# Performance work log

Measured on AMD Instinct MI355X. Metric: run time of the kernel, lower is better.

The kernel has to match this reference:

```python
import jax, jax.numpy as jnp
import numpy as np

# ---- module constants (from init_kwargs / zounds.SR22050) ----
SEQ = 64
N_SAMPLES = 16384
N_EVENTS = 16
N_HARM = 32
NOISE_WS = 512
NOISE_STEP = 256
NYQ = 11025.0  # SR22050 nyquist
MIN_F0 = 20.0 / NYQ
MAX_F0 = 800.0 / NYQ
F0_DIFF = MAX_F0 - MIN_F0
HARM_FACTOR = jnp.arange(2, 2 + N_HARM, dtype=jnp.float32)  # [2..33]


def lin_interp(x, size):
    """torch F.interpolate(mode='linear', align_corners=False) along last dim."""
    L = x.shape[-1]
    pos = (jnp.arange(size, dtype=x.dtype) + 0.5) * (L / size) - 0.5
    pos = jnp.clip(pos, 0.0, L - 1)
    i0 = jnp.floor(pos).astype(jnp.int32)
    i1 = jnp.minimum(i0 + 1, L - 1)
    w = (pos - i0).astype(x.dtype)
    return x[..., i0] * (1.0 - w) + x[..., i1] * w


def band_filtered_noise(noise_frames, mean, std):
    """Per-frame Gaussian band-pass of white noise in the STFT domain, overlap-add.
    noise_frames: (b,e,F,ws); mean/std: (b,e,F) in normalized freq [0,1]."""
    ws = noise_frames.shape[-1]
    n = jnp.arange(ws, dtype=noise_frames.dtype)
    win = 0.5 - 0.5 * jnp.cos(2.0 * jnp.pi * n / ws)  # Hann
    spec = jnp.fft.rfft(noise_frames * win, axis=-1)  # (b,e,F,ws//2+1)
    freqs = jnp.linspace(0.0, 1.0, ws // 2 + 1)
    filt = jnp.exp(-0.5 * ((freqs[None, None, None, :] - mean[..., None]) / std[..., None]) ** 2)
    frames = jnp.fft.irfft(spec * filt, n=ws, axis=-1)  # (b,e,F,ws)
    # overlap-add with hop NOISE_STEP (ws == 2*step -> two half-chunks per frame)
    b, e, Fn, _ = frames.shape
    chunks = frames.reshape(b, e, Fn, 2, NOISE_STEP)
    a = chunks[..., 0, :].reshape(b, e, Fn * NOISE_STEP)
    c = chunks[..., 1, :].reshape(b, e, Fn * NOISE_STEP)
    out = jnp.zeros((b, e, (Fn + 1) * NOISE_STEP), dtype=frames.dtype)
    out = out.at[..., : Fn * NOISE_STEP].add(a)
    out = out.at[..., NOISE_STEP:].add(c)
    return out[..., :N_SAMPLES]


def setup_inputs() -> dict:
    key = jax.random.key(0)
    ks = jax.random.split(key, 8)
    B = 8
    return {
        "f0": jax.random.uniform(ks[0], (B, N_EVENTS, SEQ), jnp.float32),
        "overall_env": jax.random.uniform(ks[1], (B, N_EVENTS, SEQ), jnp.float32),
        "osc_env": jax.random.uniform(ks[2], (B, N_EVENTS, SEQ), jnp.float32),
        "noise_env": jax.random.uniform(ks[3], (B, N_EVENTS, SEQ), jnp.float32),
        "harm_env": jax.random.uniform(ks[4], (B, N_EVENTS, N_HARM, SEQ), jnp.float32),
        "noise_std": jax.random.uniform(ks[5], (B, N_EVENTS, SEQ), jnp.float32),
        "f0_baselines": jax.random.uniform(ks[6], (B, N_EVENTS, 1), jnp.float32),
        "noise_frames": jax.random.normal(ks[7], (B, N_EVENTS, SEQ, NOISE_WS), jnp.float32),
    }


def reference(f0, overall_env, osc_env, noise_env, harm_env, noise_std, f0_baselines, noise_frames):
    # f0_baselines branch (ERB-scaled deviation around baseline)
    f0 = jnp.clip(f0, -0.5, 0.5)
    scaled_erb = (0.108 * (f0_baselines * NYQ) + 24.7) / NYQ
    f0 = f0_baselines + f0 * scaled_erb

    orig_f0 = f0 = jnp.clip(f0, 0.0, 1.0)
    overall_env = jnp.clip(overall_env, 0.0, 1.0)
    osc_env = jnp.clip(osc_env, 0.0, 1.0)
    harm_env = jnp.clip(harm_env, 0.0, 1.0)
    noise_std = jnp.clip(noise_std, 1e-12, 1.0)

    f0n = MIN_F0 + f0 * F0_DIFF                                   # (b,e,S)
    harm_f = f0n[:, :, None, :] * HARM_FACTOR[None, None, :, None]  # (b,e,H,S)
    harm_env = osc_env[:, :, None, :] * harm_env                  # (b,e,H,S)

    fund = lin_interp(f0n, N_SAMPLES)           # (b,e,N)
    harm_f_i = lin_interp(harm_f, N_SAMPLES)    # (b,e,H,N)
    osc_env_i = lin_interp(osc_env, N_SAMPLES)  # (b,e,N)
    harm_env_i = lin_interp(harm_env, N_SAMPLES)

    fundamental = jnp.sin(jnp.cumsum(fund * jnp.pi, axis=-1)) * osc_env_i
    harmonics = (jnp.sin(jnp.cumsum(harm_f_i * jnp.pi, axis=-1)) * harm_env_i).sum(axis=-2)
    osc = fundamental + harmonics

    noise_mean = MIN_F0 + orig_f0 * F0_DIFF
    nstd = noise_std * F0_DIFF
    noise = band_filtered_noise(noise_frames, noise_mean, nstd)

    osc_mix = lin_interp(overall_env, N_SAMPLES)
    noise_mix = lin_interp(1.0 - overall_env, N_SAMPLES)
    return osc * osc_mix + noise * noise_mix
```

## Files before the change

### kernel.cpp

```cpp
#include <hip/hip_runtime.h>
#include <math.h>

#define SEQ 64
#define NSAMP 16384
#define NHARM 32
#define NWS 512
#define NSTEP 256
#define BE 128
#define NFRAMES 8192

typedef _Float16 half8 __attribute__((ext_vector_type(8)));
typedef float f32x4 __attribute__((ext_vector_type(4)));

__device__ __forceinline__ float sin_rev(float x) {
  float r; asm("v_sin_f32 %0, %1" : "=v"(r) : "v"(x)); return r;
}
__device__ __forceinline__ float cos_rev(float x) {
  float r; asm("v_cos_f32 %0, %1" : "=v"(r) : "v"(x)); return r;
}
__device__ __forceinline__ float clip01(float v) { return fminf(fmaxf(v, 0.0f), 1.0f); }

__device__ __forceinline__ float f0_to_norm(float f0v, float bl) {
  const float NYQ = 11025.0f;
  const float MIN_F0 = 20.0f / 11025.0f;
  const float F0_DIFF = 780.0f / 11025.0f;
  float v = fminf(fmaxf(f0v, -0.5f), 0.5f);
  float erb = (0.108f * (bl * NYQ) + 24.7f) / NYQ;
  float fv = clip01(bl + v * erb);
  return MIN_F0 + fv * F0_DIFF;
}

__global__ __launch_bounds__(256) void prep_k(_Float16* __restrict__ W1) {
  const int m = blockIdx.x, k = m & 127;
  const int tid = threadIdx.x;
  const bool isSin = m >= 128;
  for (int n = tid; n < 512; n += 256) {
    int a = (k * n) & 511;
    float ph = (float)a * (1.0f / 512.0f);
    W1[m * 512 + n] = (_Float16)(isSin ? sin_rev(ph) : cos_rev(ph));
  }
}

__global__ __launch_bounds__(256) void gemmf_k(const float* __restrict__ Af,
                                               const _Float16* __restrict__ B,
                                               _Float16* __restrict__ Cout,
                                               _Float16* __restrict__ W2,
                                               const float* __restrict__ f0,
                                               const float* __restrict__ nstd,
                                               const float* __restrict__ f0b) {
  const int tid = threadIdx.x;

  if (blockIdx.x < 256) {
    const int k = tid & 127;
    const bool isSin = tid >= 128;
#pragma unroll
    for (int rr = 0; rr < 2; ++rr) {
      const int n = blockIdx.x * 2 + rr;
      int a = (k * n) & 511;
      float ph = (float)a * (1.0f / 512.0f);
      W2[n * 256 + tid] = (_Float16)(isSin ? sin_rev(ph) : cos_rev(ph));
    }
    return;
  }

  const int p = blockIdx.x - 256;
  const int x = p & 7, j = p >> 3;
  const int mstripe = ((j >> 2) << 3) + x;
  const int bn0 = (j & 3) * 64;
  const int m0 = mstripe * 64;

  const int Kt = 512;
  const int wave = tid >> 6, lane = tid & 63;
  const int r = lane & 15, q = lane >> 4;
  __shared__ __align__(16) _Float16 Ash[2][64 * 64];
  __shared__ __align__(16) _Float16 Bsh[2][64 * 64];
  __shared__ __align__(16) float whann[512];

  const int nT = Kt >> 6;
  const int srow0 = tid >> 3, srow1 = (256 + tid) >> 3;
  const int skg = tid & 7;

  half8 ra[2], rb[2];
  f32x4 acc[4] = {};

  whann[tid] = 0.5f - 0.5f * cos_rev((float)tid * (1.0f / 512.0f));
  whann[tid + 256] = 0.5f - 0.5f * cos_rev((float)(tid + 256) * (1.0f / 512.0f));
  __syncthreads();

  auto load_a = [&](int kk) {
    const float* s0 = Af + (size_t)(m0 + srow0) * Kt + kk + skg * 8;
    const float* s1 = Af + (size_t)(m0 + srow1) * Kt + kk + skg * 8;
    float4 a0 = ((const float4*)s0)[0], a1 = ((const float4*)s0)[1];
    float4 b0 = ((const float4*)s1)[0], b1 = ((const float4*)s1)[1];
    float4 w0 = *(const float4*)(&whann[kk + skg * 8]);
    float4 w1 = *(const float4*)(&whann[kk + skg * 8 + 4]);
    ra[0][0] = (_Float16)(a0.x * w0.x); ra[0][1] = (_Float16)(a0.y * w0.y);
    ra[0][2] = (_Float16)(a0.z * w0.z); ra[0][3] = (_Float16)(a0.w * w0.w);
    ra[0][4] = (_Float16)(a1.x * w1.x); ra[0][5] = (_Float16)(a1.y * w1.y);
    ra[0][6] = (_Float16)(a1.z * w1.z); ra[0][7] = (_Float16)(a1.w * w1.w);
    ra[1][0] = (_Float16)(b0.x * w0.x); ra[1][1] = (_Float16)(b0.y * w0.y);
    ra[1][2] = (_Float16)(b0.z * w0.z); ra[1][3] = (_Float16)(b0.w * w0.w);
    ra[1][4] = (_Float16)(b1.x * w1.x); ra[1][5] = (_Float16)(b1.y * w1.y);
    ra[1][6] = (_Float16)(b1.z * w1.z); ra[1][7] = (_Float16)(b1.w * w1.w);
    rb[0] = *(const half8*)(B + (size_t)(bn0 + srow0) * Kt + kk + skg * 8);
    rb[1] = *(const half8*)(B + (size_t)(bn0 + srow1) * Kt + kk + skg * 8);
  };
  auto store_lds = [&](int b) {
    *(half8*)(&Ash[b][srow0 * 64 + ((skg ^ (srow0 & 7)) << 3)]) = ra[0];
    *(half8*)(&Ash[b][srow1 * 64 + ((skg ^ (srow1 & 7)) << 3)]) = ra[1];
    *(half8*)(&Bsh[b][srow0 * 64 + ((skg ^ (srow0 & 7)) << 3)]) = rb[0];
    *(half8*)(&Bsh[b][srow1 * 64 + ((skg ^ (srow1 & 7)) << 3)]) = rb[1];
  };

  load_a(0);
  store_lds(0);

  for (int t = 0;;) {
    if (t + 1 < nT) load_a((t + 1) << 6);
    __syncthreads();
    const int b = t & 1;
#pragma unroll
    for (int ks = 0; ks < 2; ++ks) {
      const int swz = ((ks * 4 + q) ^ (r & 7)) << 3;
      half8 af = *(const half8*)(&Ash[b][(wave * 16 + r) * 64 + swz]);
      half8 bf0 = *(const half8*)(&Bsh[b][(0 * 16 + r) * 64 + swz]);
      half8 bf1 = *(const half8*)(&Bsh[b][(1 * 16 + r) * 64 + swz]);
      half8 bf2 = *(const half8*)(&Bsh[b][(2 * 16 + r) * 64 + swz]);
      half8 bf3 = *(const half8*)(&Bsh[b][(3 * 16 + r) * 64 + swz]);
      acc[0] = __builtin_amdgcn_mfma_f32_16x16x32_f16(af, bf0, acc[0], 0, 0, 0);
      acc[1] = __builtin_amdgcn_mfma_f32_16x16x32_f16(af, bf1, acc[1], 0, 0, 0);
      acc[2] = __builtin_amdgcn_mfma_f32_16x16x32_f16(af, bf2, acc[2], 0, 0, 0);
      acc[3] = __builtin_amdgcn_mfma_f32_16x16x32_f16(af, bf3, acc[3], 0, 0, 0);
    }
    if (t + 1 >= nT) break;
    __syncthreads();
    store_lds((t + 1) & 1);
    ++t;
  }

  const float F0_DIFF = 780.0f / 11025.0f;
#pragma unroll
  for (int reg = 0; reg < 4; ++reg) {
    const int row = m0 + wave * 16 + q * 4 + reg;
    const float mu = f0_to_norm(f0[row], f0b[row >> 6]);
    const float sd = fminf(fmaxf(nstd[row], 1e-12f), 1.0f) * F0_DIFF;
    const float inv_sd = 1.0f / sd;
    const float a = inv_sd * (1.0f / 256.0f);
    const float bmu = mu * inv_sd;
#pragma unroll
    for (int ni = 0; ni < 4; ++ni) {
      const int col = bn0 + ni * 16 + r;
      const int k = col & 127;
      float z = fmaf((float)k, a, -bmu);
      float cf = (k == 0) ? (1.0f / 512.0f) : (2.0f / 512.0f);
      float s = cf * exp2f(z * z * -0.72134752044f);
      Cout[(size_t)row * 256 + col] = (_Float16)(acc[ni][reg] * s);
    }
  }
}

__global__ __launch_bounds__(256) void invfin_k(const _Float16* __restrict__ AB,
                                                const _Float16* __restrict__ W2,
                                                const float* __restrict__ f0,
                                                const float* __restrict__ f0b,
                                                const float* __restrict__ oenv_g,
                                                const float* __restrict__ oscenv_g,
                                                const float* __restrict__ henv_g,
                                                float* __restrict__ out) {
  const int p = blockIdx.x;
  const int x = p & 7, j = p >> 3;
  const int be = ((j >> 2) << 3) + x;
  const int n0 = (j & 3) * 64;
  const int m0 = be * 64;
  const int tid = threadIdx.x;
  const int wave = tid >> 6, lane = tid & 63;
  const int r = lane & 15, q = lane >> 4;

  __shared__ __align__(16) _Float16 Ash[65 * 64];
  __shared__ __align__(16) _Float16 B1sh[64 * 64];
  __shared__ __align__(16) _Float16 B2sh[64 * 64];
  __shared__ __align__(16) float4 qe4[8 * SEQ];
  __shared__ float oenv[SEQ], oscE[SEQ];
  __shared__ float Fs[SEQ], Ds[SEQ], Gs[SEQ];

  if (tid < SEQ) {
    oenv[tid] = clip01(oenv_g[be * SEQ + tid]);
    oscE[tid] = clip01(oscenv_g[be * SEQ + tid]);
    Fs[tid] = f0_to_norm(f0[be * SEQ + tid], f0b[be]);
  }
  __syncthreads();

  if (tid < SEQ) {
    const int s = tid;
    float fcur = Fs[s];
    float fnxt = (s < 63) ? Fs[s + 1] : Fs[63];
    Ds[s] = fnxt - fcur;
    double term = 128.0 * ((double)fcur + (double)fnxt);
    double sc = term;
#pragma unroll
    for (int off = 1; off < 64; off <<= 1) {
      double u = __shfl_up(sc, off, 64);
      if (s >= off) sc += u;
    }
    double C = 128.0 * (double)Fs[0] + (sc - term);
    Gs[s] = (float)(C - 2.0 * floor(C * 0.5));
  }

  for (int idx = tid; idx < 8 * SEQ; idx += 256) {
    int hq = idx >> 6, s = idx & 63;
    const float* hb = henv_g + (size_t)be * (NHARM * SEQ) + (4 * hq) * SEQ + s;
    float e = oscE[s];
    qe4[idx] = make_float4(e * clip01(hb[0]), e * clip01(hb[64]),
                           e * clip01(hb[128]), e * clip01(hb[192]));
  }

  auto stage_AB = [&](int kk) {
#pragma unroll
    for (int it = 0; it < 3; ++it) {
      int g = it * 256 + tid;
      if (g < 520) {
        int row = g >> 3, kg = g & 7;
        half8 v = {0, 0, 0, 0, 0, 0, 0, 0};
        if (row > 0)
          v = *(const half8*)(AB + (size_t)(m0 - 1 + row) * 256 + kk + kg * 8);
        *(half8*)(&Ash[row * 64 + ((kg ^ (row & 7)) << 3)]) = v;
      }
    }
#pragma unroll
    for (int it = 0; it < 4; ++it) {
      int g = it * 256 + tid;
      int row = (g >> 3) & 63, kg = g & 7;
      bool second = g >= 512;
      int wrow = n0 + row + (second ? 256 : 0);
      half8 v = *(const half8*)(W2 + (size_t)wrow * 256 + kk + kg * 8);
      _Float16* dst = second ? B2sh : B1sh;
      *(half8*)(&dst[row * 64 + ((kg ^ (row & 7)) << 3)]) = v;
    }
  };

  f32x4 acc[4] = {};
  stage_AB(0);
  __syncthreads();

  for (int t = 0;;) {
#pragma unroll
    for (int ks = 0; ks < 2; ++ks) {
      const int kg = ks * 4 + q;
      const int ra1 = 1 + wave * 16 + r;
      const int ra2 = wave * 16 + r;
      half8 af1 = *(const half8*)(&Ash[ra1 * 64 + ((kg ^ (ra1 & 7)) << 3)]);
      half8 af2 = *(const half8*)(&Ash[ra2 * 64 + ((kg ^ (ra2 & 7)) << 3)]);
#pragma unroll
      for (int ni = 0; ni < 4; ++ni) {
        const int rb = ni * 16 + r;
        const int sw = (kg ^ (rb & 7)) << 3;
        half8 bf1 = *(const half8*)(&B1sh[rb * 64 + sw]);
        half8 bf2 = *(const half8*)(&B2sh[rb * 64 + sw]);
        acc[ni] = __builtin_amdgcn_mfma_f32_16x16x32_f16(af1, bf1, acc[ni], 0, 0, 0);
        acc[ni] = __builtin_amdgcn_mfma_f32_16x16x32_f16(af2, bf2, acc[ni], 0, 0, 0);
      }
    }
    if (t == 3) break;
    __syncthreads();
    stage_AB((t + 1) << 6);
    __syncthreads();
    ++t;
  }

#pragma unroll
  for (int reg = 0; reg < 4; ++reg) {
    const int c = wave * 16 + q * 4 + reg;
#pragma unroll
    for (int ni = 0; ni < 4; ++ni) {
      const int n = n0 + ni * 16 + r;
      const int t = c * 256 + n;
      float pos = ((float)t + 0.5f) * (1.0f / 256.0f) - 0.5f;
      pos = fminf(fmaxf(pos, 0.0f), 63.0f);
      int i0 = (int)pos;
      int i1 = min(i0 + 1, 63);
      float w = pos - (float)i0;

      float pph;
      if (t < 128) {
        pph = (float)(t + 1) * Fs[0];
      } else {
        int s = (t - 128) >> 8;
        float u1 = (float)((t - 128) - (s << 8) + 1);
        pph = Gs[s] + fmaf(Ds[s] * (1.0f / 512.0f), u1 * u1, u1 * Fs[s]);
      }
      pph = pph - 2.0f * floorf(pph * 0.5f);
      float xv = pph * 0.5f;
      float sb = sin_rev(xv);
      float cb = cos_rev(xv);
      float C = 2.0f * cb;

      float fund = sb * (oscE[i0] * (1.0f - w) + oscE[i1] * w);
      float d0 = 0.0f, d1 = 0.0f;
      float sp = sb;
      float scur = C * sb;
#pragma unroll
      for (int hq = 0; hq < 8; ++hq) {
        float4 qa = qe4[hq * 64 + i0];
        float4 qb = qe4[hq * 64 + i1];
        d0 = fmaf(scur, qa.x, d0); d1 = fmaf(scur, qb.x, d1);
        sp = fmaf(C, scur, -sp);
        d0 = fmaf(sp, qa.y, d0);   d1 = fmaf(sp, qb.y, d1);
        scur = fmaf(C, sp, -scur);
        d0 = fmaf(scur, qa.z, d0); d1 = fmaf(scur, qb.z, d1);
        sp = fmaf(C, scur, -sp);
        d0 = fmaf(sp, qa.w, d0);   d1 = fmaf(sp, qb.w, d1);
        scur = fmaf(C, sp, -scur);
      }
      float osc = fund + d0 * (1.0f - w) + d1 * w;
      float mix = oenv[i0] * (1.0f - w) + oenv[i1] * w;
      out[(size_t)be * NSAMP + t] = fmaf(osc, mix, acc[ni][reg] * (1.0f - mix));
    }
  }
}

extern "C" void kernel_launch(void* const* d_in, const int* in_sizes, int n_in,
                              void* d_out, int out_size, void* d_ws, size_t ws_size,
                              hipStream_t stream) {
  const float* f0           = (const float*)d_in[0];
  const float* overall_env  = (const float*)d_in[1];
  const float* osc_env      = (const float*)d_in[2];
  const float* harm_env     = (const float*)d_in[4];
  const float* noise_std    = (const float*)d_in[5];
  const float* f0_base      = (const float*)d_in[6];
  const float* noise_frames = (const float*)d_in[7];
  float* out = (float*)d_out;

  _Float16* W1 = (_Float16*)d_ws;
  _Float16* W2 = W1 + 256 * 512;
  _Float16* AB = W2 + 512 * 256;

  prep_k<<<256, 256, 0, stream>>>(W1);
  gemmf_k<<<768, 256, 0, stream>>>(noise_frames, W1, AB, W2, f0, noise_std, f0_base);
  invfin_k<<<512, 256, 0, stream>>>(
      AB, W2, f0, f0_base, overall_env, osc_env, harm_env, out);
}
```

Baseline: 36.95 us.

## Fuse three kernels into one monolithic kernel with on-the-fly DFT twiddles

Replaces the prep, forward-DFT GEMM and inverse/finalize kernels with a single kernel in which each block handles 8 output chunks plus a halo frame. The forward spectrum is kept in shared memory instead of a global intermediate. DFT twiddle factors are generated in registers with hardware sin/cos rather than loaded from precomputed tables. This removes two launches and the global round-trips, but adds much transcendental work per MFMA and recomputes the halo frame, and the M dimension of each 16-row MFMA tile is only partly used (10 of 16 rows).

```diff
diff --git a/kernel.cpp b/kernel.cpp
--- a/kernel.cpp
+++ b/kernel.cpp
@@ -4,8 +4,6 @@
 #define SEQ 64
 #define NSAMP 16384
 #define NHARM 32
-#define NWS 512
-#define NSTEP 256
 #define BE 128
 #define NFRAMES 8192
 
@@ -30,163 +28,42 @@
   return MIN_F0 + fv * F0_DIFF;
 }
 
-__global__ __launch_bounds__(256) void prep_k(_Float16* __restrict__ W1) {
-  const int m = blockIdx.x, k = m & 127;
-  const int tid = threadIdx.x;
-  const bool isSin = m >= 128;
-  for (int n = tid; n < 512; n += 256) {
-    int a = (k * n) & 511;
-    float ph = (float)a * (1.0f / 512.0f);
-    W1[m * 512 + n] = (_Float16)(isSin ? sin_rev(ph) : cos_rev(ph));
-  }
-}
-
-__global__ __launch_bounds__(256) void gemmf_k(const float* __restrict__ Af,
-                                               const _Float16* __restrict__ B,
-                                               _Float16* __restrict__ Cout,
-                                               _Float16* __restrict__ W2,
-                                               const float* __restrict__ f0,
-                                               const float* __restrict__ nstd,
-                                               const float* __restrict__ f0b) {
-  const int tid = threadIdx.x;
-
-  if (blockIdx.x < 256) {
-    const int k = tid & 127;
-    const bool isSin = tid >= 128;
-#pragma unroll
-    for (int rr = 0; rr < 2; ++rr) {
-      const int n = blockIdx.x * 2 + rr;
-      int a = (k * n) & 511;
-      float ph = (float)a * (1.0f / 512.0f);
-      W2[n * 256 + tid] = (_Float16)(isSin ? sin_rev(ph) : cos_rev(ph));
-    }
-    return;
-  }
-
-  const int p = blockIdx.x - 256;
-  const int x = p & 7, j = p >> 3;
-  const int mstripe = ((j >> 2) << 3) + x;
-  const int bn0 = (j & 3) * 64;
-  const int m0 = mstripe * 64;
-
-  const int Kt = 512;
-  const int wave = tid >> 6, lane = tid & 63;
-  const int r = lane & 15, q = lane >> 4;
-  __shared__ __align__(16) _Float16 Ash[2][64 * 64];
-  __shared__ __align__(16) _Float16 Bsh[2][64 * 64];
+__global__ __launch_bounds__(256, 4) void mono_k(
+    const float* __restrict__ Af,
+    const float* __restrict__ f0,
+    const float* __restrict__ nstd,
+    const float* __restrict__ f0b,
+    const float* __restrict__ oenv_g,
+    const float* __restrict__ oscenv_g,
+    const float* __restrict__ henv_g,
+    float* __restrict__ out) {
+  __shared__ __align__(16) _Float16 A_all[10 * 512];
+  __shared__ __align__(16) _Float16 ABl[10 * 256];
   __shared__ __align__(16) float whann[512];
-
-  const int nT = Kt >> 6;
-  const int srow0 = tid >> 3, srow1 = (256 + tid) >> 3;
-  const int skg = tid & 7;
-
-  half8 ra[2], rb[2];
-  f32x4 acc[4] = {};
-
-  whann[tid] = 0.5f - 0.5f * cos_rev((float)tid * (1.0f / 512.0f));
-  whann[tid + 256] = 0.5f - 0.5f * cos_rev((float)(tid + 256) * (1.0f / 512.0f));
-  __syncthreads();
-
-  auto load_a = [&](int kk) {
-    const float* s0 = Af + (size_t)(m0 + srow0) * Kt + kk + skg * 8;
-    const float* s1 = Af + (size_t)(m0 + srow1) * Kt + kk + skg * 8;
-    float4 a0 = ((const float4*)s0)[0], a1 = ((const float4*)s0)[1];
-    float4 b0 = ((const float4*)s1)[0], b1 = ((const float4*)s1)[1];
-    float4 w0 = *(const float4*)(&whann[kk + skg * 8]);
-    float4 w1 = *(const float4*)(&whann[kk + skg * 8 + 4]);
-    ra[0][0] = (_Float16)(a0.x * w0.x); ra[0][1] = (_Float16)(a0.y * w0.y);
-    ra[0][2] = (_Float16)(a0.z * w0.z); ra[0][3] = (_Float16)(a0.w * w0.w);
-    ra[0][4] = (_Float16)(a1.x * w1.x); ra[0][5] = (_Float16)(a1.y * w1.y);
-    ra[0][6] = (_Float16)(a1.z * w1.z); ra[0][7] = (_Float16)(a1.w * w1.w);
-    ra[1][0] = (_Float16)(b0.x * w0.x); ra[1][1] = (_Float16)(b0.y * w0.y);
-    ra[1][2] = (_Float16)(b0.z * w0.z); ra[1][3] = (_Float16)(b0.w * w0.w);
-    ra[1][4] = (_Float16)(b1.x * w1.x); ra[1][5] = (_Float16)(b1.y * w1.y);
-    ra[1][6] = (_Float16)(b1.z * w1.z); ra[1][7] = (_Float16)(b1.w * w1.w);
-    rb[0] = *(const half8*)(B + (size_t)(bn0 + srow0) * Kt + kk + skg * 8);
-    rb[1] = *(const half8*)(B + (size_t)(bn0 + srow1) * Kt + kk + skg * 8);
-  };
-  auto store_lds = [&](int b) {
-    *(half8*)(&Ash[b][srow0 * 64 + ((skg ^ (srow0 & 7)) << 3)]) = ra[0];
-    *(half8*)(&Ash[b][srow1 * 64 + ((skg ^ (srow1 & 7)) << 3)]) = ra[1];
-    *(half8*)(&Bsh[b][srow0 * 64 + ((skg ^ (srow0 & 7)) << 3)]) = rb[0];
-    *(half8*)(&Bsh[b][srow1 * 64 + ((skg ^ (srow1 & 7)) << 3)]) = rb[1];
-  };
-
-  load_a(0);
-  store_lds(0);
-
-  for (int t = 0;;) {
-    if (t + 1 < nT) load_a((t + 1) << 6);
-    __syncthreads();
-    const int b = t & 1;
-#pragma unroll
-    for (int ks = 0; ks < 2; ++ks) {
-      const int swz = ((ks * 4 + q) ^ (r & 7)) << 3;
-      half8 af = *(const half8*)(&Ash[b][(wave * 16 + r) * 64 + swz]);
-      half8 bf0 = *(const half8*)(&Bsh[b][(0 * 16 + r) * 64 + swz]);
-      half8 bf1 = *(const half8*)(&Bsh[b][(1 * 16 + r) * 64 + swz]);
-      half8 bf2 = *(const half8*)(&Bsh[b][(2 * 16 + r) * 64 + swz]);
-      half8 bf3 = *(const half8*)(&Bsh[b][(3 * 16 + r) * 64 + swz]);
-      acc[0] = __builtin_amdgcn_mfma_f32_16x16x32_f16(af, bf0, acc[0], 0, 0, 0);
-      acc[1] = __builtin_amdgcn_mfma_f32_16x16x32_f16(af, bf1, acc[1], 0, 0, 0);
-      acc[2] = __builtin_amdgcn_mfma_f32_16x16x32_f16(af, bf2, acc[2], 0, 0, 0);
-      acc[3] = __builtin_amdgcn_mfma_f32_16x16x32_f16(af, bf3, acc[3], 0, 0, 0);
-    }
-    if (t + 1 >= nT) break;
-    __syncthreads();
-    store_lds((t + 1) & 1);
-    ++t;
-  }
-
-  const float F0_DIFF = 780.0f / 11025.0f;
-#pragma unroll
-  for (int reg = 0; reg < 4; ++reg) {
-    const int row = m0 + wave * 16 + q * 4 + reg;
-    const float mu = f0_to_norm(f0[row], f0b[row >> 6]);
-    const float sd = fminf(fmaxf(nstd[row], 1e-12f), 1.0f) * F0_DIFF;
-    const float inv_sd = 1.0f / sd;
-    const float a = inv_sd * (1.0f / 256.0f);
-    const float bmu = mu * inv_sd;
-#pragma unroll
-    for (int ni = 0; ni < 4; ++ni) {
-      const int col = bn0 + ni * 16 + r;
-      const int k = col & 127;
-      float z = fmaf((float)k, a, -bmu);
-      float cf = (k == 0) ? (1.0f / 512.0f) : (2.0f / 512.0f);
-      float s = cf * exp2f(z * z * -0.72134752044f);
-      Cout[(size_t)row * 256 + col] = (_Float16)(acc[ni][reg] * s);
-    }
-  }
-}
-
-__global__ __launch_bounds__(256) void invfin_k(const _Float16* __restrict__ AB,
-                                                const _Float16* __restrict__ W2,
-                                                const float* __restrict__ f0,
-                                                const float* __restrict__ f0b,
-                                                const float* __restrict__ oenv_g,
-                                                const float* __restrict__ oscenv_g,
-                                                const float* __restrict__ henv_g,
-                                                float* __restrict__ out) {
+  __shared__ __align__(16) float4 qe4[8 * SEQ];
+  __shared__ float oenv[SEQ], oscE[SEQ], Fs[SEQ], Ds[SEQ], Gs[SEQ];
+
   const int p = blockIdx.x;
-  const int x = p & 7, j = p >> 3;
-  const int be = ((j >> 2) << 3) + x;
-  const int n0 = (j & 3) * 64;
-  const int m0 = be * 64;
+  const int be = p >> 3, qc = p & 7;
+  const int c0 = be * 64 + qc * 8;
   const int tid = threadIdx.x;
   const int wave = tid >> 6, lane = tid & 63;
   const int r = lane & 15, q = lane >> 4;
-
-  __shared__ __align__(16) _Float16 Ash[65 * 64];
-  __shared__ __align__(16) _Float16 B1sh[64 * 64];
-  __shared__ __align__(16) _Float16 B2sh[64 * 64];
-  __shared__ __align__(16) float4 qe4[8 * SEQ];
-  __shared__ float oenv[SEQ], oscE[SEQ];
-  __shared__ float Fs[SEQ], Ds[SEQ], Gs[SEQ];
-
+  const int wc = wave * 64;
+
+  whann[tid] = 0.5f - 0.5f * cos_rev((float)tid * (1.0f / 512.0f));
+  whann[tid + 256] = 0.5f - 0.5f * cos_rev((float)(tid + 256) * (1.0f / 512.0f));
   if (tid < SEQ) {
     oenv[tid] = clip01(oenv_g[be * SEQ + tid]);
     oscE[tid] = clip01(oscenv_g[be * SEQ + tid]);
     Fs[tid] = f0_to_norm(f0[be * SEQ + tid], f0b[be]);
+  }
+  for (int idx = tid; idx < 8 * SEQ; idx += 256) {
+    int hq = idx >> 6, s = idx & 63;
+    const float* hb = henv_g + (size_t)be * (NHARM * SEQ) + (4 * hq) * SEQ + s;
+    float e = clip01(oscenv_g[be * SEQ + s]);
+    qe4[idx] = make_float4(e * clip01(hb[0]), e * clip01(hb[64]),
+                           e * clip01(hb[128]), e * clip01(hb[192]));
   }
   __syncthreads();
 
@@ -205,115 +82,163 @@
     double C = 128.0 * (double)Fs[0] + (sc - term);
     Gs[s] = (float)(C - 2.0 * floor(C * 0.5));
   }
-
-  for (int idx = tid; idx < 8 * SEQ; idx += 256) {
-    int hq = idx >> 6, s = idx & 63;
-    const float* hb = henv_g + (size_t)be * (NHARM * SEQ) + (4 * hq) * SEQ + s;
-    float e = oscE[s];
-    qe4[idx] = make_float4(e * clip01(hb[0]), e * clip01(hb[64]),
-                           e * clip01(hb[128]), e * clip01(hb[192]));
-  }
-
-  auto stage_AB = [&](int kk) {
-#pragma unroll
-    for (int it = 0; it < 3; ++it) {
-      int g = it * 256 + tid;
-      if (g < 520) {
-        int row = g >> 3, kg = g & 7;
-        half8 v = {0, 0, 0, 0, 0, 0, 0, 0};
-        if (row > 0)
-          v = *(const half8*)(AB + (size_t)(m0 - 1 + row) * 256 + kk + kg * 8);
-        *(half8*)(&Ash[row * 64 + ((kg ^ (row & 7)) << 3)]) = v;
-      }
-    }
-#pragma unroll
-    for (int it = 0; it < 4; ++it) {
-      int g = it * 256 + tid;
-      int row = (g >> 3) & 63, kg = g & 7;
-      bool second = g >= 512;
-      int wrow = n0 + row + (second ? 256 : 0);
-      half8 v = *(const half8*)(W2 + (size_t)wrow * 256 + kk + kg * 8);
-      _Float16* dst = second ? B2sh : B1sh;
-      *(half8*)(&dst[row * 64 + ((kg ^ (row & 7)) << 3)]) = v;
-    }
-  };
-
-  f32x4 acc[4] = {};
-  stage_AB(0);
+  for (int g = tid; g < 640; g += 256) {
+    int row = g >> 6, kg = g & 63;
+    half8 v = {0, 0, 0, 0, 0, 0, 0, 0};
+    if (row < 9) {
+      int fi = max(c0 - 1 + row, 0);
+      const float* s0 = Af + (size_t)fi * 512 + kg * 8;
+      float4 a0 = ((const float4*)s0)[0], a1 = ((const float4*)s0)[1];
+      float4 w0 = *(const float4*)(&whann[kg * 8]);
+      float4 w1 = *(const float4*)(&whann[kg * 8 + 4]);
+      v[0] = (_Float16)(a0.x * w0.x); v[1] = (_Float16)(a0.y * w0.y);
+      v[2] = (_Float16)(a0.z * w0.z); v[3] = (_Float16)(a0.w * w0.w);
+      v[4] = (_Float16)(a1.x * w1.x); v[5] = (_Float16)(a1.y * w1.y);
+      v[6] = (_Float16)(a1.z * w1.z); v[7] = (_Float16)(a1.w * w1.w);
+    }
+    *(half8*)(&A_all[row * 512 + ((kg ^ (row & 7)) << 3)]) = v;
+  }
   __syncthreads();
 
-  for (int t = 0;;) {
-#pragma unroll
-    for (int ks = 0; ks < 2; ++ks) {
-      const int kg = ks * 4 + q;
-      const int ra1 = 1 + wave * 16 + r;
-      const int ra2 = wave * 16 + r;
-      half8 af1 = *(const half8*)(&Ash[ra1 * 64 + ((kg ^ (ra1 & 7)) << 3)]);
-      half8 af2 = *(const half8*)(&Ash[ra2 * 64 + ((kg ^ (ra2 & 7)) << 3)]);
+  {
+    f32x4 acc[4] = {};
+    int kW[4]; bool isS[4];
+#pragma unroll
+    for (int ni = 0; ni < 4; ++ni) {
+      int kap = wc + ni * 16 + r;
+      kW[ni] = kap & 127;
+      isS[ni] = kap >= 128;
+    }
+    const int arow = min(r, 9);
+    for (int u = 0; u < 16; ++u) {
+      int g = u * 4 + q;
+      half8 af = *(const half8*)(&A_all[arow * 512 + ((g ^ (arow & 7)) << 3)]);
+      int nb = u * 32 + q * 8;
 #pragma unroll
       for (int ni = 0; ni < 4; ++ni) {
-        const int rb = ni * 16 + r;
-        const int sw = (kg ^ (rb & 7)) << 3;
-        half8 bf1 = *(const half8*)(&B1sh[rb * 64 + sw]);
-        half8 bf2 = *(const half8*)(&B2sh[rb * 64 + sw]);
-        acc[ni] = __builtin_amdgcn_mfma_f32_16x16x32_f16(af1, bf1, acc[ni], 0, 0, 0);
-        acc[ni] = __builtin_amdgcn_mfma_f32_16x16x32_f16(af2, bf2, acc[ni], 0, 0, 0);
-      }
-    }
-    if (t == 3) break;
-    __syncthreads();
-    stage_AB((t + 1) << 6);
-    __syncthreads();
-    ++t;
-  }
-
-#pragma unroll
-  for (int reg = 0; reg < 4; ++reg) {
-    const int c = wave * 16 + q * 4 + reg;
-#pragma unroll
-    for (int ni = 0; ni < 4; ++ni) {
-      const int n = n0 + ni * 16 + r;
-      const int t = c * 256 + n;
-      float pos = ((float)t + 0.5f) * (1.0f / 256.0f) - 0.5f;
-      pos = fminf(fmaxf(pos, 0.0f), 63.0f);
-      int i0 = (int)pos;
-      int i1 = min(i0 + 1, 63);
-      float w = pos - (float)i0;
-
-      float pph;
-      if (t < 128) {
-        pph = (float)(t + 1) * Fs[0];
-      } else {
-        int s = (t - 128) >> 8;
-        float u1 = (float)((t - 128) - (s << 8) + 1);
-        pph = Gs[s] + fmaf(Ds[s] * (1.0f / 512.0f), u1 * u1, u1 * Fs[s]);
-      }
-      pph = pph - 2.0f * floorf(pph * 0.5f);
-      float xv = pph * 0.5f;
-      float sb = sin_rev(xv);
-      float cb = cos_rev(xv);
-      float C = 2.0f * cb;
-
-      float fund = sb * (oscE[i0] * (1.0f - w) + oscE[i1] * w);
-      float d0 = 0.0f, d1 = 0.0f;
-      float sp = sb;
-      float scur = C * sb;
-#pragma unroll
-      for (int hq = 0; hq < 8; ++hq) {
-        float4 qa = qe4[hq * 64 + i0];
-        float4 qb = qe4[hq * 64 + i1];
-        d0 = fmaf(scur, qa.x, d0); d1 = fmaf(scur, qb.x, d1);
-        sp = fmaf(C, scur, -sp);
-        d0 = fmaf(sp, qa.y, d0);   d1 = fmaf(sp, qb.y, d1);
-        scur = fmaf(C, sp, -scur);
-        d0 = fmaf(scur, qa.z, d0); d1 = fmaf(scur, qb.z, d1);
-        sp = fmaf(C, scur, -sp);
-        d0 = fmaf(sp, qa.w, d0);   d1 = fmaf(sp, qb.w, d1);
-        scur = fmaf(C, sp, -scur);
-      }
-      float osc = fund + d0 * (1.0f - w) + d1 * w;
-      float mix = oenv[i0] * (1.0f - w) + oenv[i1] * w;
-      out[(size_t)be * NSAMP + t] = fmaf(osc, mix, acc[ni][reg] * (1.0f - mix));
+        half8 bf;
+#pragma unroll
+        for (int jj = 0; jj < 8; ++jj) {
+          int a = (kW[ni] * (nb + jj)) & 511;
+          float ph = (float)a * (1.0f / 512.0f);
+          bf[jj] = (_Float16)(isS[ni] ? sin_rev(ph) : cos_rev(ph));
+        }
+        acc[ni] = __builtin_amdgcn_mfma_f32_16x16x32_f16(af, bf, acc[ni], 0, 0, 0);
+      }
+    }
+    const float F0_DIFF = 780.0f / 11025.0f;
+#pragma unroll
+    for (int reg = 0; reg < 4; ++reg) {
+      const int row = q * 4 + reg;
+      if (row <= 9) {
+        const int fi = max(c0 - 1 + row, 0);
+        const float mu = f0_to_norm(f0[fi], f0b[fi >> 6]);
+        const float sd = fminf(fmaxf(nstd[fi], 1e-12f), 1.0f) * F0_DIFF;
+        const float inv_sd = 1.0f / sd;
+        const float a = inv_sd * (1.0f / 256.0f);
+        const float bmu = mu * inv_sd;
+#pragma unroll
+        for (int ni = 0; ni < 4; ++ni) {
+          const int col = wc + ni * 16 + r;
+          const int k = col & 127;
+          float z = fmaf((float)k, a, -bmu);
+          float cf = (k == 0) ? (1.0f / 512.0f) : (2.0f / 512.0f);
+          float s = cf * exp2f(z * z * -0.72134752044f);
+          _Float16 val = (_Float16)(acc[ni][reg] * s);
+          if ((qc == 0 && row == 0) || row == 9) val = (_Float16)0.0f;
+          int colg = col >> 3;
+          ABl[row * 256 + ((colg ^ (row & 7)) << 3) + (col & 7)] = val;
+        }
+      }
+    }
+  }
+  __syncthreads();
+
+  {
+    f32x4 acc2[4] = {};
+    const int a1row = min(1 + r, 9);
+    const int a2row = min(r, 9);
+    int nB[4];
+#pragma unroll
+    for (int ni = 0; ni < 4; ++ni) nB[ni] = wc + ni * 16 + r;
+    for (int u = 0; u < 8; ++u) {
+      int gg = u * 4 + q;
+      half8 af1 = *(const half8*)(&ABl[a1row * 256 + ((gg ^ (a1row & 7)) << 3)]);
+      half8 af2 = *(const half8*)(&ABl[a2row * 256 + ((gg ^ (a2row & 7)) << 3)]);
+      int kb = u * 32 + q * 8;
+#pragma unroll
+      for (int ni = 0; ni < 4; ++ni) {
+        half8 bf1, bf2;
+#pragma unroll
+        for (int jj = 0; jj < 8; ++jj) {
+          int kap = kb + jj;
+          int k = kap & 127;
+          float ph1 = (float)((k * nB[ni]) & 511) * (1.0f / 512.0f);
+          float ph2 = (float)((k * (nB[ni] + 256)) & 511) * (1.0f / 512.0f);
+          if (kap >= 128) {
+            bf1[jj] = (_Float16)sin_rev(ph1);
+            bf2[jj] = (_Float16)sin_rev(ph2);
+          } else {
+            bf1[jj] = (_Float16)cos_rev(ph1);
+            bf2[jj] = (_Float16)cos_rev(ph2);
+          }
+        }
+        acc2[ni] = __builtin_amdgcn_mfma_f32_16x16x32_f16(af1, bf1, acc2[ni], 0, 0, 0);
+        acc2[ni] = __builtin_amdgcn_mfma_f32_16x16x32_f16(af2, bf2, acc2[ni], 0, 0, 0);
+      }
+    }
+
+#pragma unroll
+    for (int reg = 0; reg < 4; ++reg) {
+      const int crow = q * 4 + reg;
+      if (crow < 8) {
+        const int c = qc * 8 + crow;
+#pragma unroll
+        for (int ni = 0; ni < 4; ++ni) {
+          const int n = wc + ni * 16 + r;
+          const int t = c * 256 + n;
+          float pos = ((float)t + 0.5f) * (1.0f / 256.0f) - 0.5f;
+          pos = fminf(fmaxf(pos, 0.0f), 63.0f);
+          int i0 = (int)pos;
+          int i1 = min(i0 + 1, 63);
+          float w = pos - (float)i0;
+
+          float pph;
+          if (t < 128) {
+            pph = (float)(t + 1) * Fs[0];
+          } else {
+            int s = (t - 128) >> 8;
+            float u1 = (float)((t - 128) - (s << 8) + 1);
+            pph = Gs[s] + fmaf(Ds[s] * (1.0f / 512.0f), u1 * u1, u1 * Fs[s]);
+          }
+          pph = pph - 2.0f * floorf(pph * 0.5f);
+          float xv = pph * 0.5f;
+          float sb = sin_rev(xv);
+          float cb = cos_rev(xv);
+          float C = 2.0f * cb;
+
+          float fund = sb * (oscE[i0] * (1.0f - w) + oscE[i1] * w);
+          float d0 = 0.0f, d1 = 0.0f;
+          float sp = sb;
+          float scur = C * sb;
+#pragma unroll
+          for (int hq = 0; hq < 8; ++hq) {
+            float4 qa = qe4[hq * 64 + i0];
+            float4 qb = qe4[hq * 64 + i1];
+            d0 = fmaf(scur, qa.x, d0); d1 = fmaf(scur, qb.x, d1);
+            sp = fmaf(C, scur, -sp);
+            d0 = fmaf(sp, qa.y, d0);   d1 = fmaf(sp, qb.y, d1);
+            scur = fmaf(C, sp, -scur);
+            d0 = fmaf(scur, qa.z, d0); d1 = fmaf(scur, qb.z, d1);
+            sp = fmaf(C, scur, -sp);
+            d0 = fmaf(sp, qa.w, d0);   d1 = fmaf(sp, qb.w, d1);
+            scur = fmaf(C, sp, -scur);
+          }
+          float osc = fund + d0 * (1.0f - w) + d1 * w;
+          float mix = oenv[i0] * (1.0f - w) + oenv[i1] * w;
+          out[(size_t)be * NSAMP + t] = fmaf(osc, mix, acc2[ni][reg] * (1.0f - mix));
+        }
+      }
     }
   }
 }
@@ -330,12 +255,6 @@
   const float* noise_frames = (const float*)d_in[7];
   float* out = (float*)d_out;
 
-  _Float16* W1 = (_Float16*)d_ws;
-  _Float16* W2 = W1 + 256 * 512;
-  _Float16* AB = W2 + 512 * 256;
-
-  prep_k<<<256, 256, 0, stream>>>(W1);
-  gemmf_k<<<768, 256, 0, stream>>>(noise_frames, W1, AB, W2, f0, noise_std, f0_base);
-  invfin_k<<<512, 256, 0, stream>>>(
-      AB, W2, f0, f0_base, overall_env, osc_env, harm_env, out);
-}
+  mono_k<<<1024, 256, 0, stream>>>(
+      noise_frames, f0, noise_std, f0_base, overall_env, osc_env, harm_env, out);
+}
```

Measured after the change: 83.28 us. 125% more time.
